# Performance work log

Measured on AMD Instinct MI355X. Metric: run time of the kernel, lower is better.

The kernel has to match this reference:

```python
import jax, jax.numpy as jnp
import numpy as np

B = 32        # graphs per batch
MAXN = 2048   # max nodes per graph (dense batch length)
HEADS = 8
DH = 64       # head dim (512/8)
M = 256       # FAVOR+ random features
D = 512
EPS = 1e-5    # batchnorm eps
KEPS = 1e-6   # performer stabilizer


def _batchnorm(x, g, b):
    # torch BatchNorm1d training-mode: biased batch statistics over node dim
    mu = jnp.mean(x, axis=0)
    var = jnp.mean((x - mu) ** 2, axis=0)
    return (x - mu) * jax.lax.rsqrt(var + EPS) * g + b


def setup_inputs() -> dict:
    key = jax.random.key(0)
    ks = jax.random.split(key, 10)
    sizes = 1024 + (np.arange(B) * 131) % 1025   # ragged graph sizes in [1024, 2048]
    N = int(sizes.sum())                          # 48544
    E = N * 8
    batch = jnp.asarray(np.repeat(np.arange(B), sizes), dtype=jnp.int32)
    edge_index = jax.random.randint(ks[0], (2, E), 0, N, dtype=jnp.int32)
    s = 1.0 / np.sqrt(D)
    return {
        'x': jax.random.normal(ks[1], (N, D), jnp.float32),
        'batch': batch,
        'edge_index': edge_index,
        'norm1_g': jnp.ones((D,), jnp.float32),
        'norm1_b': jnp.zeros((D,), jnp.float32),
        'norm2_g': jnp.ones((D,), jnp.float32),
        'norm2_b': jnp.zeros((D,), jnp.float32),
        'W_conv': jax.random.normal(ks[2], (D, D), jnp.float32) * s,
        'b_conv': jnp.zeros((D,), jnp.float32),
        'Wq': jax.random.normal(ks[3], (D, D), jnp.float32) * s,
        'Wk': jax.random.normal(ks[4], (D, D), jnp.float32) * s,
        'Wv': jax.random.normal(ks[5], (D, D), jnp.float32) * s,
        'Wo': jax.random.normal(ks[6], (D, D), jnp.float32) * s,
        'proj': jax.random.normal(ks[7], (M, DH), jnp.float32),
    }


def _forward(x, batch, edge_index, norm1_g, norm1_b, norm2_g, norm2_b,
             W_conv, b_conv, Wq, Wk, Wv, Wo, proj):
    N = x.shape[0]
    E = edge_index.shape[1]
    h = x

    # norm1 (+ dropout p=0 -> identity) then local GNN conv (mean-agg GCN + linear + relu)
    xn = _batchnorm(x, norm1_g, norm1_b)
    msg = xn[edge_index[0]]                                        # [E, D] gather
    agg = jax.ops.segment_sum(msg, edge_index[1], num_segments=N)  # [N, D] scatter-add
    deg = jax.ops.segment_sum(jnp.ones((E,), x.dtype), edge_index[1], num_segments=N)
    agg = agg / jnp.maximum(deg, 1.0)[:, None]
    conv_out = jax.nn.relu(agg @ W_conv + b_conv)

    # to_dense_batch(h, batch) -> h_dense [B, MAXN, D], mask [B, MAXN]
    counts = jax.ops.segment_sum(jnp.ones((N,), jnp.int32), batch, num_segments=B)
    offsets = jnp.concatenate([jnp.zeros((1,), jnp.int32), jnp.cumsum(counts)[:-1]])
    pos = jnp.arange(N, dtype=jnp.int32) - offsets[batch]
    h_dense = jnp.zeros((B, MAXN, D), x.dtype).at[batch, pos].set(h)
    mask = jnp.zeros((B, MAXN), bool).at[batch, pos].set(True)

    # Performer FAVOR+ non-causal self-attention
    def heads(t, W):
        return (t @ W).reshape(B, MAXN, HEADS, DH).transpose(0, 2, 1, 3)  # [B,H,MAXN,DH]
    q, k, v = heads(h_dense, Wq), heads(h_dense, Wk), heads(h_dense, Wv)

    scale = DH ** -0.25  # data normalizer applied to q and k each

    def phi(t, is_query):
        t = t * scale
        u = jnp.einsum('bhnd,md->bhnm', t, proj)           # [B,H,MAXN,M]
        diag = 0.5 * jnp.sum(t * t, axis=-1, keepdims=True)
        if is_query:
            m_ = jnp.max(u, axis=-1, keepdims=True)
        else:
            m_ = jnp.max(u, axis=(-2, -1), keepdims=True)
        return jnp.exp(u - diag - jax.lax.stop_gradient(m_)) / np.sqrt(M) + KEPS

    qf = phi(q, True)
    kf = phi(k, False) * mask[:, None, :, None]   # zero padded keys
    vm = v * mask[:, None, :, None]

    kv = jnp.einsum('bhnm,bhnd->bhmd', kf, vm)                    # [B,H,M,DH]
    z = 1.0 / (jnp.einsum('bhnm,bhm->bhn', qf, kf.sum(axis=2)) + KEPS)
    attn = jnp.einsum('bhnm,bhmd->bhnd', qf, kv) * z[..., None]   # [B,H,MAXN,DH]
    attn = attn.transpose(0, 2, 1, 3).reshape(B, MAXN, D) @ Wo

    h_attn = attn[batch, pos]                                      # gather back: [mask]

    return _batchnorm(conv_out + h_attn + h, norm2_g, norm2_b)


def reference(x, batch, edge_index, norm1_g, norm1_b, norm2_g, norm2_b,
              W_conv, b_conv, Wq, Wk, Wv, Wo, proj):
    return _forward(x, batch, edge_index, norm1_g, norm1_b, norm2_g, norm2_b,
                    W_conv, b_conv, Wq, Wk, Wv, Wo, proj)
```

## Files before the change

### kernel.cpp

```cpp
#include <hip/hip_runtime.h>
#include <stdint.h>

#define CDIV(a,b) (((a)+(b)-1)/(b))

typedef __attribute__((ext_vector_type(4))) float f32x4;
typedef __attribute__((ext_vector_type(8))) short s16x8;
typedef __attribute__((ext_vector_type(8))) unsigned short u16x8;
typedef __attribute__((ext_vector_type(4))) unsigned short u16x4;

__device__ __forceinline__ float bf2f(unsigned short u) {
  union { unsigned int i; float f; } c; c.i = ((unsigned int)u) << 16; return c.f;
}
__device__ __forceinline__ unsigned short f2bf(float f) {
  union { float f; unsigned int i; } c; c.f = f;
  unsigned int u = c.i;
  u += 0x7fffu + ((u >> 16) & 1u);
  return (unsigned short)(u >> 16);
}

template<int BM, int BN, int WM, int WN, int EPI>
__global__ __launch_bounds__(256) void gemm_bt(
    const unsigned short* __restrict__ A, const unsigned short* __restrict__ B,
    void* __restrict__ Cout, const float* __restrict__ aux,
    int K, int lda, int ldb, int ldc, long zsC, int Mstore)
{
  constexpr int MT = BM / (WM * 16);
  constexpr int NT = BN / (WN * 16);
  constexpr int LDT = 40;
  __shared__ unsigned short As[BM * LDT];
  __shared__ unsigned short Bs[BN * LDT];
  const int tid = threadIdx.x, wid = tid >> 6, lane = tid & 63;
  const int wr = wid / WN, wc = wid % WN;
  long m0 = (long)blockIdx.y * BM;
  const int n0 = blockIdx.x * BN;
  f32x4 acc[MT][NT] = {};
  for (int k0 = 0; k0 < K; k0 += 32) {
    #pragma unroll
    for (int c = tid; c < BM * 4; c += 256) {
      int row = c >> 2, c8 = (c & 3) * 8;
      *(u16x8*)(&As[row * LDT + c8]) = *(const u16x8*)(A + (m0 + row) * lda + k0 + c8);
    }
    #pragma unroll
    for (int c = tid; c < BN * 4; c += 256) {
      int row = c >> 2, c8 = (c & 3) * 8;
      *(u16x8*)(&Bs[row * LDT + c8]) = *(const u16x8*)(B + (long)(n0 + row) * ldb + k0 + c8);
    }
    __syncthreads();
    s16x8 af[MT], bfv[NT];
    #pragma unroll
    for (int mt = 0; mt < MT; mt++)
      af[mt] = *(const s16x8*)(&As[(wr * MT * 16 + mt * 16 + (lane & 15)) * LDT + ((lane >> 4) * 8)]);
    #pragma unroll
    for (int nt = 0; nt < NT; nt++)
      bfv[nt] = *(const s16x8*)(&Bs[(wc * NT * 16 + nt * 16 + (lane & 15)) * LDT + ((lane >> 4) * 8)]);
    #pragma unroll
    for (int mt = 0; mt < MT; mt++)
      #pragma unroll
      for (int nt = 0; nt < NT; nt++)
        acc[mt][nt] = __builtin_amdgcn_mfma_f32_16x16x32_bf16(af[mt], bfv[nt], acc[mt][nt], 0, 0, 0);
    __syncthreads();
  }
  #pragma unroll
  for (int mt = 0; mt < MT; mt++) {
    const int rl0 = wr * (MT * 16) + mt * 16 + ((lane >> 4) << 2);
    #pragma unroll
    for (int nt = 0; nt < NT; nt++) {
      const int col = n0 + wc * (NT * 16) + nt * 16 + (lane & 15);
      #pragma unroll
      for (int i = 0; i < 4; i++) {
        long r = m0 + rl0 + i;
        if (r < Mstore) {
          float v = acc[mt][nt][i];
          long ci = r * ldc + col;
          if constexpr (EPI == 5) {
            float o = v + aux[col];
            o = o > 0.f ? o : 0.f;
            ((float*)Cout)[ci] += o;
          } else if constexpr (EPI == 7) {
            ((unsigned short*)Cout)[(long)(col >> 6) * zsC + r * 64 + (col & 63)] = f2bf(v);
          } else if constexpr (EPI == 8) {
            ((float*)Cout)[ci] = v + aux[ci];
          }
        }
      }
    }
  }
}

__global__ __launch_bounds__(256) void k_kmax(
    const unsigned short* __restrict__ kvqh, const unsigned short* __restrict__ projb,
    const unsigned int* __restrict__ offs, unsigned int* __restrict__ kmax, long Npad) {
  __shared__ float wmax[4];
  const int tid = threadIdx.x, wid = tid >> 6, lane = tid & 63;
  const int b = blockIdx.y, h = blockIdx.z;
  const unsigned int off = offs[b];
  const int nb = (int)(offs[b + 1] - off);
  const int m0 = blockIdx.x * 64;
  if (m0 >= nb) return;
  const unsigned short* A = kvqh + ((long)(8 + h) * Npad + off + m0) * 64;
  f32x4 acc[4][4] = {};
  #pragma unroll
  for (int k0 = 0; k0 < 64; k0 += 32) {
    s16x8 af[4], bfv[4];
    #pragma unroll
    for (int mt = 0; mt < 4; mt++)
      af[mt] = *(const s16x8*)(A + (long)(mt * 16 + (lane & 15)) * 64 + k0 + ((lane >> 4) * 8));
    #pragma unroll
    for (int nt = 0; nt < 4; nt++)
      bfv[nt] = *(const s16x8*)(projb + (long)(wid * 64 + nt * 16 + (lane & 15)) * 64 + k0 + ((lane >> 4) * 8));
    #pragma unroll
    for (int mt = 0; mt < 4; mt++)
      #pragma unroll
      for (int nt = 0; nt < 4; nt++)
        acc[mt][nt] = __builtin_amdgcn_mfma_f32_16x16x32_bf16(af[mt], bfv[nt], acc[mt][nt], 0, 0, 0);
  }
  float bm = -3.0e38f;
  #pragma unroll
  for (int mt = 0; mt < 4; mt++)
    #pragma unroll
    for (int i = 0; i < 4; i++) {
      int row = mt * 16 + ((lane >> 4) << 2) + i;
      if (m0 + row < nb) {
        #pragma unroll
        for (int nt = 0; nt < 4; nt++) bm = fmaxf(bm, acc[mt][nt][i]);
      }
    }
  #pragma unroll
  for (int s = 1; s < 64; s <<= 1) bm = fmaxf(bm, __shfl_xor(bm, s));
  if (lane == 0) wmax[wid] = bm;
  __syncthreads();
  if (tid == 0) {
    float m = fmaxf(fmaxf(wmax[0], wmax[1]), fmaxf(wmax[2], wmax[3]));
    atomicMax(&kmax[b * 8 + h], __float_as_uint(fmaxf(m, 0.f)));
  }
}

__global__ __launch_bounds__(256) void k_kvm(
    const unsigned short* __restrict__ kvqh, const unsigned short* __restrict__ projb,
    const unsigned int* __restrict__ offs, const unsigned int* __restrict__ kmax,
    unsigned short* __restrict__ kvTb, float* __restrict__ kfsum, long Npad) {
  constexpr int TLD = 72;
  __shared__ unsigned short vsT[2][64 * TLD];
  __shared__ unsigned short kfsT[64 * TLD];
  const int tid = threadIdx.x, wid = tid >> 6, lane = tid & 63;
  const int mblk = blockIdx.x, b = blockIdx.y, h = blockIdx.z;
  const unsigned int off = offs[b];
  const int nb = (int)(offs[b + 1] - off);
  const float km = __uint_as_float(kmax[b * 8 + h]);
  const unsigned short* Kp = kvqh + ((long)(8 + h) * Npad + off) * 64;
  const unsigned short* Vp = kvqh + ((long)(16 + h) * Npad + off) * 64;
  const unsigned short* Pp = projb + (long)(mblk * 64 + wid * 16) * 64;
  const int l15 = lane & 15, hi = lane >> 4;
  const int mloc = wid * 16 + l15;

  #pragma unroll
  for (int c = tid; c < 512; c += 256) {
    int row = c >> 3, c8 = (c & 7) * 8;
    int rot = (c & 7) * 8;
    u16x8 v = *(const u16x8*)(Vp + (long)row * 64 + c8);
    #pragma unroll
    for (int j = 0; j < 8; j++) vsT[0][(c8 + j) * TLD + ((row + rot) & 63)] = v[j];
  }
  __syncthreads();

  f32x4 akv[4] = {};
  float ksum = 0.f;
  int buf = 0;
  for (int n0 = 0; n0 < nb; n0 += 64) {
    f32x4 acc[4] = {};
    float dsum[4] = {0.f, 0.f, 0.f, 0.f};
    #pragma unroll
    for (int k0 = 0; k0 < 64; k0 += 32) {
      s16x8 af[4];
      #pragma unroll
      for (int mt = 0; mt < 4; mt++)
        af[mt] = *(const s16x8*)(Kp + ((long)n0 + mt * 16 + l15) * 64 + k0 + hi * 8);
      s16x8 bfv = *(const s16x8*)(Pp + (long)l15 * 64 + k0 + hi * 8);
      #pragma unroll
      for (int mt = 0; mt < 4; mt++) {
        #pragma unroll
        for (int j = 0; j < 8; j++) {
          float a = bf2f((unsigned short)af[mt][j]);
          dsum[mt] += a * a;
        }
        acc[mt] = __builtin_amdgcn_mfma_f32_16x16x32_bf16(af[mt], bfv, acc[mt], 0, 0, 0);
      }
    }
    float rs[4];
    #pragma unroll
    for (int mt = 0; mt < 4; mt++) {
      float s = dsum[mt];
      s += __shfl_xor(s, 16); s += __shfl_xor(s, 32);
      rs[mt] = 0.0625f * s;
    }
    #pragma unroll
    for (int mt = 0; mt < 4; mt++) {
      int r0 = mt * 16 + hi * 4;
      float e[4];
      #pragma unroll
      for (int i = 0; i < 4; i++) {
        float dg = __shfl(rs[mt], hi * 4 + i);
        e[i] = (n0 + r0 + i < nb) ? (__expf(acc[mt][i] - dg - km) * 0.0625f + 1e-6f) : 0.f;
      }
      ksum += e[0] + e[1] + e[2] + e[3];
      unsigned int p0 = (unsigned int)f2bf(e[0]) | ((unsigned int)f2bf(e[1]) << 16);
      unsigned int p1 = (unsigned int)f2bf(e[2]) | ((unsigned int)f2bf(e[3]) << 16);
      *(unsigned int*)(&kfsT[mloc * TLD + r0]) = p0;
      *(unsigned int*)(&kfsT[mloc * TLD + r0 + 2]) = p1;
    }
    if (n0 + 64 < nb) {
      #pragma unroll
      for (int c = tid; c < 512; c += 256) {
        int row = c >> 3, c8 = (c & 7) * 8;
        int rot = (c & 7) * 8;
        u16x8 v = *(const u16x8*)(Vp + ((long)n0 + 64 + row) * 64 + c8);
        #pragma unroll
        for (int j = 0; j < 8; j++) vsT[buf ^ 1][(c8 + j) * TLD + ((row + rot) & 63)] = v[j];
      }
    }
    #pragma unroll
    for (int ks = 0; ks < 2; ks++) {
      s16x8 bB = *(const s16x8*)(&kfsT[mloc * TLD + ks * 32 + hi * 8]);
      #pragma unroll
      for (int mt2 = 0; mt2 < 4; mt2++) {
        int d = mt2 * 16 + l15;
        int rrot = ((ks * 32 + hi * 8) + ((d >> 3) & 7) * 8) & 63;
        s16x8 aA = *(const s16x8*)(&vsT[buf][d * TLD + rrot]);
        akv[mt2] = __builtin_amdgcn_mfma_f32_16x16x32_bf16(aA, bB, akv[mt2], 0, 0, 0);
      }
    }
    __syncthreads();
    buf ^= 1;
  }
  long base = ((long)b * 8 + h) * 16384;
  const int m = mblk * 64 + mloc;
  #pragma unroll
  for (int mt2 = 0; mt2 < 4; mt2++)
    #pragma unroll
    for (int i = 0; i < 4; i++) {
      int d = mt2 * 16 + hi * 4 + i;
      kvTb[base + (long)d * 256 + m] = f2bf(akv[mt2][i]);
    }
  ksum += __shfl_xor(ksum, 16); ksum += __shfl_xor(ksum, 32);
  if (hi == 0) kfsum[((long)b * 8 + h) * 256 + m] = ksum;
}

__global__ __launch_bounds__(256) void k_qflash(
    const unsigned short* __restrict__ qh_all, const unsigned short* __restrict__ projb,
    const unsigned short* __restrict__ kvTb, const float* __restrict__ kfsum,
    const unsigned int* __restrict__ offs, unsigned short* __restrict__ attn, long Npad) {
  constexpr int QLDT = 264;
  __shared__ unsigned short qfs[64 * QLDT];
  __shared__ float skf[256];
  __shared__ float sdiag[64];
  __shared__ float smax[4][64];
  __shared__ float szp[4][64];
  const int tid = threadIdx.x, wid = tid >> 6, lane = tid & 63;
  const int b = blockIdx.y, h = blockIdx.z;
  const unsigned int off = offs[b];
  const int nb = (int)(offs[b + 1] - off);
  const int m0 = blockIdx.x * 64;
  if (m0 >= nb) return;
  const unsigned short* A = qh_all + ((long)h * Npad + off + m0) * 64;
  skf[tid] = kfsum[((long)b * 8 + h) * 256 + tid];
  f32x4 acc[4][4] = {};
  float dsum[4] = {0.f, 0.f, 0.f, 0.f};
  #pragma unroll
  for (int k0 = 0; k0 < 64; k0 += 32) {
    s16x8 af[4], bfv[4];
    #pragma unroll
    for (int mt = 0; mt < 4; mt++)
      af[mt] = *(const s16x8*)(A + (long)(mt * 16 + (lane & 15)) * 64 + k0 + ((lane >> 4) * 8));
    #pragma unroll
    for (int nt = 0; nt < 4; nt++)
      bfv[nt] = *(const s16x8*)(projb + (long)(wid * 64 + nt * 16 + (lane & 15)) * 64 + k0 + ((lane >> 4) * 8));
    if (wid == 0) {
      #pragma unroll
      for (int mt = 0; mt < 4; mt++)
        #pragma unroll
        for (int j = 0; j < 8; j++) {
          float a = bf2f((unsigned short)af[mt][j]);
          dsum[mt] += a * a;
        }
    }
    #pragma unroll
    for (int mt = 0; mt < 4; mt++)
      #pragma unroll
      for (int nt = 0; nt < 4; nt++)
        acc[mt][nt] = __builtin_amdgcn_mfma_f32_16x16x32_bf16(af[mt], bfv[nt], acc[mt][nt], 0, 0, 0);
  }
  if (wid == 0) {
    #pragma unroll
    for (int mt = 0; mt < 4; mt++) {
      float s = dsum[mt];
      s += __shfl_xor(s, 16); s += __shfl_xor(s, 32);
      if (lane < 16) sdiag[mt * 16 + lane] = 0.0625f * s;
    }
  }
  #pragma unroll
  for (int mt = 0; mt < 4; mt++)
    #pragma unroll
    for (int i = 0; i < 4; i++) {
      float rm = fmaxf(fmaxf(acc[mt][0][i], acc[mt][1][i]), fmaxf(acc[mt][2][i], acc[mt][3][i]));
      rm = fmaxf(rm, __shfl_xor(rm, 1)); rm = fmaxf(rm, __shfl_xor(rm, 2));
      rm = fmaxf(rm, __shfl_xor(rm, 4)); rm = fmaxf(rm, __shfl_xor(rm, 8));
      if ((lane & 15) == 0) smax[wid][mt * 16 + ((lane >> 4) << 2) + i] = rm;
    }
  __syncthreads();
  #pragma unroll
  for (int mt = 0; mt < 4; mt++)
    #pragma unroll
    for (int i = 0; i < 4; i++) {
      int row = mt * 16 + ((lane >> 4) << 2) + i;
      float rm = fmaxf(fmaxf(smax[0][row], smax[1][row]), fmaxf(smax[2][row], smax[3][row]));
      float dg = sdiag[row];
      float zp = 0.f;
      #pragma unroll
      for (int nt = 0; nt < 4; nt++) {
        int col = wid * 64 + nt * 16 + (lane & 15);
        float e = __expf(acc[mt][nt][i] - dg - rm) * 0.0625f + 1e-6f;
        qfs[row * QLDT + col] = f2bf(e);
        zp += e * skf[col];
      }
      zp += __shfl_xor(zp, 1); zp += __shfl_xor(zp, 2);
      zp += __shfl_xor(zp, 4); zp += __shfl_xor(zp, 8);
      if ((lane & 15) == 0) szp[wid][row] = zp;
    }
  __syncthreads();
  const unsigned short* kvb = kvTb + ((long)b * 8 + h) * 16384;
  f32x4 acc2[4] = {};
  #pragma unroll
  for (int ks = 0; ks < 8; ks++) {
    s16x8 aq = *(const s16x8*)(&qfs[(wid * 16 + (lane & 15)) * QLDT + ks * 32 + ((lane >> 4) * 8)]);
    #pragma unroll
    for (int ntd = 0; ntd < 4; ntd++) {
      s16x8 bk = *(const s16x8*)(kvb + (long)(ntd * 16 + (lane & 15)) * 256 + ks * 32 + ((lane >> 4) * 8));
      acc2[ntd] = __builtin_amdgcn_mfma_f32_16x16x32_bf16(aq, bk, acc2[ntd], 0, 0, 0);
    }
  }
  #pragma unroll
  for (int ntd = 0; ntd < 4; ntd++)
    #pragma unroll
    for (int i = 0; i < 4; i++) {
      int row = wid * 16 + ((lane >> 4) << 2) + i;
      if (m0 + row < nb) {
        float zr = 1.f / (szp[0][row] + szp[1][row] + szp[2][row] + szp[3][row] + 1e-6f);
        attn[(long)(off + m0 + row) * 512 + h * 64 + ntd * 16 + (lane & 15)] = f2bf(acc2[ntd][i] * zr);
      }
    }
}


__global__ void k_fill(float* __restrict__ out, long n, float v) {
  long i = (long)blockIdx.x * 256 + threadIdx.x;
  if (i < n) out[i] = v;
}

__global__ void k_convert_x(const float* __restrict__ x, unsigned short* __restrict__ xb,
                            long ntotal, long nreal) {
  long i = ((long)blockIdx.x * 256 + threadIdx.x) * 4;
  if (i >= ntotal) return;
  u16x4 o;
  if (i < nreal) {
    f32x4 v = *(const f32x4*)(x + i);
    o[0] = f2bf(v[0]); o[1] = f2bf(v[1]); o[2] = f2bf(v[2]); o[3] = f2bf(v[3]);
  } else { o[0] = 0; o[1] = 0; o[2] = 0; o[3] = 0; }
  *(u16x4*)(xb + i) = o;
}

__global__ void k_transall(const float* __restrict__ w0, const float* __restrict__ w1,
                           const float* __restrict__ w2, const float* __restrict__ w3,
                           const float* __restrict__ w4, unsigned short* __restrict__ out) {
  long idx = (long)blockIdx.x * 256 + threadIdx.x;
  if (idx >= (5L << 18)) return;
  int which = (int)(idx >> 18);
  int r = (int)(idx & 262143);
  int n = r >> 9, k = r & 511;
  const float* w = which == 0 ? w0 : which == 1 ? w1 : which == 2 ? w2 : which == 3 ? w3 : w4;
  out[idx] = f2bf(w[k * 512 + n]);
}

__global__ void k_scale_copy_bf(const float* __restrict__ in, unsigned short* __restrict__ out,
                                int n, float scl) {
  int i = blockIdx.x * 256 + threadIdx.x;
  if (i < n) out[i] = f2bf(in[i] * scl);
}

__global__ void k_bn_stats(const float* __restrict__ x, float* __restrict__ s1,
                           float* __restrict__ s2, int N, int rpb) {
  int t = threadIdx.x;
  int r0 = blockIdx.x * rpb;
  int r1 = min(N, r0 + rpb);
  float a1 = 0, a2 = 0, b1 = 0, b2 = 0;
  for (int r = r0; r < r1; r++) {
    float va = x[(long)r * 512 + t];
    float vb = x[(long)r * 512 + t + 256];
    a1 += va; a2 += va * va; b1 += vb; b2 += vb * vb;
  }
  atomicAdd(&s1[t], a1); atomicAdd(&s2[t], a2);
  atomicAdd(&s1[t + 256], b1); atomicAdd(&s2[t + 256], b2);
}

__global__ void k_bn_final(const float* __restrict__ s1, const float* __restrict__ s2,
                           const float* __restrict__ g, const float* __restrict__ b,
                           float* __restrict__ a, float* __restrict__ c, float invN) {
  int t = threadIdx.x;
  float mu = s1[t] * invN;
  float var = s2[t] * invN - mu * mu;
  float inv = rsqrtf(var + 1e-5f);
  float av = g[t] * inv;
  a[t] = av;
  c[t] = b[t] - mu * av;
}

__global__ void k_deg(const int* __restrict__ ed, unsigned int* __restrict__ deg, long E) {
  long i = (long)blockIdx.x * 256 + threadIdx.x;
  if (i < E) atomicAdd(&deg[ed[i]], 1u);
}

__global__ void k_offs(const int* __restrict__ batch, unsigned int* __restrict__ offs, int N) {
  int i = blockIdx.x * 256 + threadIdx.x;
  if (i >= N) return;
  int b = batch[i];
  if (i == 0) { for (int bb = 0; bb <= b; bb++) offs[bb] = 0; }
  else {
    int pb = batch[i - 1];
    if (pb != b) for (int bb = pb + 1; bb <= b; bb++) offs[bb] = i;
  }
  if (i == N - 1) { for (int bb = b + 1; bb <= 32; bb++) offs[bb] = N; }
}

__global__ __launch_bounds__(1024) void k_scan_nodes(const unsigned int* __restrict__ deg,
                                                     unsigned int* __restrict__ rowstart, int N) {
  __shared__ unsigned int wsum[16];
  __shared__ unsigned int carry_s;
  int t = threadIdx.x, lane = t & 63, wid = t >> 6;
  if (t == 0) carry_s = 0;
  __syncthreads();
  for (int base = 0; base < N; base += 1024) {
    int i = base + t;
    unsigned int v = (i < N) ? deg[i] : 0;
    unsigned int sc = v;
    #pragma unroll
    for (int s = 1; s < 64; s <<= 1) {
      unsigned int u = __shfl_up(sc, s);
      if (lane >= s) sc += u;
    }
    if (lane == 63) wsum[wid] = sc;
    __syncthreads();
    unsigned int woff = 0, tot = 0;
    #pragma unroll
    for (int w = 0; w < 16; w++) { unsigned int s = wsum[w]; if (w < wid) woff += s; tot += s; }
    unsigned int carry = carry_s;
    if (i < N) rowstart[i] = carry + woff + sc - v;
    __syncthreads();
    if (t == 0) carry_s = carry + tot;
    __syncthreads();
  }
  if (threadIdx.x == 0) rowstart[N] = carry_s;
}

__global__ void k_csr_fill(const int* __restrict__ es, const int* __restrict__ ed,
                           const unsigned int* __restrict__ rowstart,
                           unsigned int* __restrict__ cursor, int* __restrict__ csr, long E) {
  long e = (long)blockIdx.x * 256 + threadIdx.x;
  if (e >= E) return;
  int d = ed[e];
  unsigned int slot = atomicAdd(&cursor[d], 1u);
  csr[rowstart[d] + slot] = es[e];
}

__global__ __launch_bounds__(128) void k_gather(const int* __restrict__ csr,
                                                const unsigned int* __restrict__ rowstart,
                                                const float* __restrict__ x,
                                                const float* __restrict__ a1, const float* __restrict__ c1,
                                                unsigned short* __restrict__ conv_in, int N) {
  long n = blockIdx.x;
  int c = threadIdx.x * 4;
  u16x4 o; o[0] = 0; o[1] = 0; o[2] = 0; o[3] = 0;
  if (n < N) {
    unsigned int r0 = rowstart[n], r1 = rowstart[n + 1];
    if (r1 > r0) {
      f32x4 acc0 = {}, acc1 = {};
      unsigned int j = r0;
      for (; j + 2 <= r1; j += 2) {
        int s0 = csr[j], s1 = csr[j + 1];
        acc0 += *(const f32x4*)(x + (long)s0 * 512 + c);
        acc1 += *(const f32x4*)(x + (long)s1 * 512 + c);
      }
      if (j < r1) { int s0 = csr[j]; acc0 += *(const f32x4*)(x + (long)s0 * 512 + c); }
      f32x4 acc = acc0 + acc1;
      float inv = 1.f / (float)(r1 - r0);
      o[0] = f2bf(acc[0] * inv * a1[c + 0] + c1[c + 0]);
      o[1] = f2bf(acc[1] * inv * a1[c + 1] + c1[c + 1]);
      o[2] = f2bf(acc[2] * inv * a1[c + 2] + c1[c + 2]);
      o[3] = f2bf(acc[3] * inv * a1[c + 3] + c1[c + 3]);
    }
  }
  *(u16x4*)(conv_in + n * 512 + c) = o;
}

__global__ void k_stats(const float* __restrict__ y, float* __restrict__ s1,
                        float* __restrict__ s2, int N, int rpb) {
  int t = threadIdx.x;
  int r0 = blockIdx.x * rpb;
  int r1 = min(N, r0 + rpb);
  float a1 = 0, a2 = 0, b1 = 0, b2 = 0;
  for (int r = r0; r < r1; r++) {
    float va = y[(long)r * 512 + t];
    float vb = y[(long)r * 512 + t + 256];
    a1 += va; a2 += va * va; b1 += vb; b2 += vb * vb;
  }
  atomicAdd(&s1[t], a1); atomicAdd(&s2[t], a2);
  atomicAdd(&s1[t + 256], b1); atomicAdd(&s2[t + 256], b2);
}

__global__ void k_bn_apply(float* __restrict__ y, const float* __restrict__ a,
                           const float* __restrict__ c, long total) {
  long i4 = ((long)blockIdx.x * 256 + threadIdx.x) * 4;
  if (i4 >= total) return;
  int col = (int)(i4 & 511);
  f32x4 v = *(const f32x4*)(y + i4);
  #pragma unroll
  for (int j = 0; j < 4; j++) v[j] = v[j] * a[col + j] + c[col + j];
  *(f32x4*)(y + i4) = v;
}


extern "C" void kernel_launch(void* const* d_in, const int* in_sizes, int n_in,
                              void* d_out, int out_size, void* d_ws, size_t ws_size,
                              hipStream_t stream) {
  (void)n_in; (void)out_size;
  const float* x = (const float*)d_in[0];
  const int* batch = (const int*)d_in[1];
  const int* eidx = (const int*)d_in[2];
  const float* n1g = (const float*)d_in[3];
  const float* n1b = (const float*)d_in[4];
  const float* n2g = (const float*)d_in[5];
  const float* n2b = (const float*)d_in[6];
  const float* wconv = (const float*)d_in[7];
  const float* bconv = (const float*)d_in[8];
  const float* wq = (const float*)d_in[9];
  const float* wk = (const float*)d_in[10];
  const float* wv = (const float*)d_in[11];
  const float* wo = (const float*)d_in[12];
  const float* proj = (const float*)d_in[13];

  const int N = in_sizes[1];
  const long E = in_sizes[2] / 2;
  const long Npad = CDIV(N, 128) * 128 + 256;
  const int Mb = (int)((CDIV(N, 128) * 128 + 128) / 128);
  const int* es = eidx;
  const int* ed = eidx + E;
  float* out = (float*)d_out;

  char* p = (char*)d_ws;
  auto alloc = [&](size_t bytes) -> char* {
    char* r = p;
    p += (bytes + 255) & ~(size_t)255;
    return r;
  };
  unsigned short* kvqh = (unsigned short*)alloc((size_t)24 * Npad * 64 * 2);
  unsigned short* xbf  = (unsigned short*)alloc((size_t)Npad * 512 * 2);
  unsigned short* kvT_b = (unsigned short*)alloc((size_t)32 * 8 * 16384 * 2);
  unsigned short* wts   = (unsigned short*)alloc((size_t)5 * 512 * 512 * 2);
  unsigned short* proj_s = (unsigned short*)alloc((size_t)256 * 64 * 2);
  float* bn1_acc = (float*)alloc(1024 * 4);
  float* bn1_ac  = (float*)alloc(1024 * 4);
  float* bn2_acc = (float*)alloc(1024 * 4);
  float* bn2_ac  = (float*)alloc(1024 * 4);
  unsigned int* deg      = (unsigned int*)alloc((size_t)N * 4);
  unsigned int* offs     = (unsigned int*)alloc(33 * 4);
  unsigned int* kmax     = (unsigned int*)alloc(32 * 8 * 4);
  float* kfsum = (float*)alloc((size_t)32 * 8 * 256 * 4);
  unsigned int* rowstart = (unsigned int*)alloc((size_t)(N + 1) * 4);
  unsigned int* cursor   = (unsigned int*)alloc((size_t)N * 4);
  int* csr               = (int*)alloc((size_t)E * 4);
  size_t required = (size_t)(p - (char*)d_ws);
  if (required > ws_size) {
    k_fill<<<(int)CDIV((long)N * 512, 256), 256, 0, stream>>>(
        out, (long)N * 512, 1.0e6f + (float)(ws_size >> 20));
    return;
  }
  unsigned short* wqkv_t  = wts;
  unsigned short* wconv_t = wts + 3 * 512 * 512;
  unsigned short* wo_t    = wts + 4 * 512 * 512;
  unsigned short* attn_all = xbf;
  unsigned short* conv_in  = xbf;

  hipMemsetAsync(deg, 0, (size_t)N * 4, stream);
  hipMemsetAsync(cursor, 0, (size_t)N * 4, stream);
  hipMemsetAsync(kmax, 0, 32 * 8 * 4, stream);
  hipMemsetAsync(bn1_acc, 0, 1024 * 4, stream);
  hipMemsetAsync(bn2_acc, 0, 1024 * 4, stream);

  k_convert_x<<<(int)CDIV(Npad * 512 / 4, 256), 256, 0, stream>>>(x, xbf, Npad * 512, (long)N * 512);
  k_transall<<<(int)CDIV(5L << 18, 256), 256, 0, stream>>>(wq, wk, wv, wconv, wo, wts);
  k_scale_copy_bf<<<CDIV(256 * 64, 256), 256, 0, stream>>>(proj, proj_s, 256 * 64, 0.35355339059327373f);

  int rpb = CDIV(N, 1024);
  k_bn_stats<<<1024, 256, 0, stream>>>(x, bn1_acc, bn1_acc + 512, N, rpb);
  k_bn_final<<<1, 512, 0, stream>>>(bn1_acc, bn1_acc + 512, n1g, n1b, bn1_ac, bn1_ac + 512, 1.f / N);
  k_deg<<<(int)CDIV(E, 256), 256, 0, stream>>>(ed, deg, E);
  k_offs<<<CDIV(N, 256), 256, 0, stream>>>(batch, offs, N);
  k_scan_nodes<<<1, 1024, 0, stream>>>(deg, rowstart, N);
  k_csr_fill<<<(int)CDIV(E, 256), 256, 0, stream>>>(es, ed, rowstart, cursor, csr, E);

  gemm_bt<128, 128, 2, 2, 7><<<dim3(12, Mb), 256, 0, stream>>>(
      xbf, wqkv_t, kvqh, nullptr, 512, 512, 512, 0, (long)Npad * 64, (int)Npad);

  k_kmax<<<dim3(32, 32, 8), 256, 0, stream>>>(kvqh, proj_s, offs, kmax, Npad);
  k_kvm<<<dim3(4, 32, 8), 256, 0, stream>>>(kvqh, proj_s, offs, kmax, kvT_b, kfsum, Npad);

  k_qflash<<<dim3(32, 32, 8), 256, 0, stream>>>(
      kvqh, proj_s, kvT_b, kfsum, offs, attn_all, Npad);

  gemm_bt<128, 128, 2, 2, 8><<<dim3(4, Mb), 256, 0, stream>>>(
      attn_all, wo_t, out, x, 512, 512, 512, 512, 0, N);

  k_gather<<<(int)(CDIV(N, 128) * 128), 128, 0, stream>>>(csr, rowstart, x, bn1_ac, bn1_ac + 512, conv_in, N);
  gemm_bt<128, 128, 2, 2, 5><<<dim3(4, Mb), 256, 0, stream>>>(
      conv_in, wconv_t, out, bconv, 512, 512, 512, 512, 0, N);

  k_stats<<<1024, 256, 0, stream>>>(out, bn2_acc, bn2_acc + 512, N, rpb);
  k_bn_final<<<1, 512, 0, stream>>>(bn2_acc, bn2_acc + 512, n2g, n2b, bn2_ac, bn2_ac + 512, 1.f / N);
  k_bn_apply<<<(int)CDIV((long)N * 512 / 4, 256), 256, 0, stream>>>(out, bn2_ac, bn2_ac + 512, (long)N * 512);
}
```

Before: 1.187 ms.

## Fuse x conversion with BN stats, fold key-sum into kv MFMA, reorder grids

The x-to-bf16 conversion now runs in the same pass as the first batchnorm statistics, so x is read once instead of twice. The separate padding-zero pass becomes a memset. The performer normaliser is computed by an extra MFMA against a key-feature-sum row stored in bf16 alongside kv, which removes the shared-memory dot product and the cross-wave reduction in k_qflash. The attention grids are flattened so that batch/head varies fastest, and the QKV GEMM uses 256-wide N tiles. Storing the key sum in bf16 costs precision in the denominator, and an extra memset clears the enlarged kv buffer.

```diff
diff --git a/kernel.cpp b/kernel.cpp
--- a/kernel.cpp
+++ b/kernel.cpp
@@ -17,6 +17,8 @@
   u += 0x7fffu + ((u >> 16) & 1u);
   return (unsigned short)(u >> 16);
 }
+
+#define KVROWS 80
 
 template<int BM, int BN, int WM, int WN, int EPI>
 __global__ __launch_bounds__(256) void gemm_bt(
@@ -92,10 +94,11 @@
     const unsigned int* __restrict__ offs, unsigned int* __restrict__ kmax, long Npad) {
   __shared__ float wmax[4];
   const int tid = threadIdx.x, wid = tid >> 6, lane = tid & 63;
-  const int b = blockIdx.y, h = blockIdx.z;
+  const int bh = blockIdx.x & 255, xb = blockIdx.x >> 8;
+  const int b = bh >> 3, h = bh & 7;
   const unsigned int off = offs[b];
   const int nb = (int)(offs[b + 1] - off);
-  const int m0 = blockIdx.x * 64;
+  const int m0 = xb * 64;
   if (m0 >= nb) return;
   const unsigned short* A = kvqh + ((long)(8 + h) * Npad + off + m0) * 64;
   f32x4 acc[4][4] = {};
@@ -138,12 +141,13 @@
 __global__ __launch_bounds__(256) void k_kvm(
     const unsigned short* __restrict__ kvqh, const unsigned short* __restrict__ projb,
     const unsigned int* __restrict__ offs, const unsigned int* __restrict__ kmax,
-    unsigned short* __restrict__ kvTb, float* __restrict__ kfsum, long Npad) {
+    unsigned short* __restrict__ kvTb, long Npad) {
   constexpr int TLD = 72;
   __shared__ unsigned short vsT[2][64 * TLD];
   __shared__ unsigned short kfsT[64 * TLD];
   const int tid = threadIdx.x, wid = tid >> 6, lane = tid & 63;
-  const int mblk = blockIdx.x, b = blockIdx.y, h = blockIdx.z;
+  const int bh = blockIdx.x & 255, mblk = blockIdx.x >> 8;
+  const int b = bh >> 3, h = bh & 7;
   const unsigned int off = offs[b];
   const int nb = (int)(offs[b + 1] - off);
   const float km = __uint_as_float(kmax[b * 8 + h]);
@@ -232,7 +236,7 @@
     __syncthreads();
     buf ^= 1;
   }
-  long base = ((long)b * 8 + h) * 16384;
+  long base = ((long)b * 8 + h) * (KVROWS * 256);
   const int m = mblk * 64 + mloc;
   #pragma unroll
   for (int mt2 = 0; mt2 < 4; mt2++)
@@ -242,27 +246,26 @@
       kvTb[base + (long)d * 256 + m] = f2bf(akv[mt2][i]);
     }
   ksum += __shfl_xor(ksum, 16); ksum += __shfl_xor(ksum, 32);
-  if (hi == 0) kfsum[((long)b * 8 + h) * 256 + m] = ksum;
+  if (hi == 0) kvTb[base + 64 * 256 + m] = f2bf(ksum);
 }
 
 __global__ __launch_bounds__(256) void k_qflash(
     const unsigned short* __restrict__ qh_all, const unsigned short* __restrict__ projb,
-    const unsigned short* __restrict__ kvTb, const float* __restrict__ kfsum,
-    const unsigned int* __restrict__ offs, unsigned short* __restrict__ attn, long Npad) {
+    const unsigned short* __restrict__ kvTb, const unsigned int* __restrict__ offs,
+    unsigned short* __restrict__ attn, long Npad) {
   constexpr int QLDT = 264;
   __shared__ unsigned short qfs[64 * QLDT];
-  __shared__ float skf[256];
   __shared__ float sdiag[64];
   __shared__ float smax[4][64];
-  __shared__ float szp[4][64];
   const int tid = threadIdx.x, wid = tid >> 6, lane = tid & 63;
-  const int b = blockIdx.y, h = blockIdx.z;
+  const int l15 = lane & 15, hi = lane >> 4;
+  const int bh = blockIdx.x & 255, xb = blockIdx.x >> 8;
+  const int b = bh >> 3, h = bh & 7;
   const unsigned int off = offs[b];
   const int nb = (int)(offs[b + 1] - off);
-  const int m0 = blockIdx.x * 64;
+  const int m0 = xb * 64;
   if (m0 >= nb) return;
   const unsigned short* A = qh_all + ((long)h * Npad + off + m0) * 64;
-  skf[tid] = kfsum[((long)b * 8 + h) * 256 + tid];
   f32x4 acc[4][4] = {};
   float dsum[4] = {0.f, 0.f, 0.f, 0.f};
   #pragma unroll
@@ -270,10 +273,10 @@
     s16x8 af[4], bfv[4];
     #pragma unroll
     for (int mt = 0; mt < 4; mt++)
-      af[mt] = *(const s16x8*)(A + (long)(mt * 16 + (lane & 15)) * 64 + k0 + ((lane >> 4) * 8));
+      af[mt] = *(const s16x8*)(A + (long)(mt * 16 + l15) * 64 + k0 + hi * 8);
     #pragma unroll
     for (int nt = 0; nt < 4; nt++)
-      bfv[nt] = *(const s16x8*)(projb + (long)(wid * 64 + nt * 16 + (lane & 15)) * 64 + k0 + ((lane >> 4) * 8));
+      bfv[nt] = *(const s16x8*)(projb + (long)(wid * 64 + nt * 16 + l15) * 64 + k0 + hi * 8);
     if (wid == 0) {
       #pragma unroll
       for (int mt = 0; mt < 4; mt++)
@@ -304,49 +307,50 @@
       float rm = fmaxf(fmaxf(acc[mt][0][i], acc[mt][1][i]), fmaxf(acc[mt][2][i], acc[mt][3][i]));
       rm = fmaxf(rm, __shfl_xor(rm, 1)); rm = fmaxf(rm, __shfl_xor(rm, 2));
       rm = fmaxf(rm, __shfl_xor(rm, 4)); rm = fmaxf(rm, __shfl_xor(rm, 8));
-      if ((lane & 15) == 0) smax[wid][mt * 16 + ((lane >> 4) << 2) + i] = rm;
+      if (l15 == 0) smax[wid][mt * 16 + hi * 4 + i] = rm;
     }
   __syncthreads();
   #pragma unroll
   for (int mt = 0; mt < 4; mt++)
     #pragma unroll
     for (int i = 0; i < 4; i++) {
-      int row = mt * 16 + ((lane >> 4) << 2) + i;
+      int row = mt * 16 + hi * 4 + i;
       float rm = fmaxf(fmaxf(smax[0][row], smax[1][row]), fmaxf(smax[2][row], smax[3][row]));
-      float dg = sdiag[row];
-      float zp = 0.f;
+      float sub = sdiag[row] + rm;
       #pragma unroll
       for (int nt = 0; nt < 4; nt++) {
-        int col = wid * 64 + nt * 16 + (lane & 15);
-        float e = __expf(acc[mt][nt][i] - dg - rm) * 0.0625f + 1e-6f;
-        qfs[row * QLDT + col] = f2bf(e);
-        zp += e * skf[col];
-      }
-      zp += __shfl_xor(zp, 1); zp += __shfl_xor(zp, 2);
-      zp += __shfl_xor(zp, 4); zp += __shfl_xor(zp, 8);
-      if ((lane & 15) == 0) szp[wid][row] = zp;
+        int col = wid * 64 + nt * 16 + l15;
+        qfs[row * QLDT + col] = f2bf(__expf(acc[mt][nt][i] - sub) * 0.0625f + 1e-6f);
+      }
     }
   __syncthreads();
-  const unsigned short* kvb = kvTb + ((long)b * 8 + h) * 16384;
+  const unsigned short* kvb = kvTb + ((long)b * 8 + h) * (KVROWS * 256);
   f32x4 acc2[4] = {};
+  f32x4 acc3 = {};
   #pragma unroll
   for (int ks = 0; ks < 8; ks++) {
-    s16x8 aq = *(const s16x8*)(&qfs[(wid * 16 + (lane & 15)) * QLDT + ks * 32 + ((lane >> 4) * 8)]);
-    #pragma unroll
-    for (int ntd = 0; ntd < 4; ntd++) {
-      s16x8 bk = *(const s16x8*)(kvb + (long)(ntd * 16 + (lane & 15)) * 256 + ks * 32 + ((lane >> 4) * 8));
-      acc2[ntd] = __builtin_amdgcn_mfma_f32_16x16x32_bf16(aq, bk, acc2[ntd], 0, 0, 0);
-    }
-  }
-  #pragma unroll
-  for (int ntd = 0; ntd < 4; ntd++)
+    s16x8 aq = *(const s16x8*)(&qfs[(wid * 16 + l15) * QLDT + ks * 32 + hi * 8]);
+    #pragma unroll
+    for (int t = 0; t < 4; t++) {
+      s16x8 bk = *(const s16x8*)(kvb + (long)(t * 16 + l15) * 256 + ks * 32 + hi * 8);
+      acc2[t] = __builtin_amdgcn_mfma_f32_16x16x32_bf16(aq, bk, acc2[t], 0, 0, 0);
+    }
+    s16x8 bz = *(const s16x8*)(kvb + (long)(64 + l15) * 256 + ks * 32 + hi * 8);
+    acc3 = __builtin_amdgcn_mfma_f32_16x16x32_bf16(aq, bz, acc3, 0, 0, 0);
+  }
+  float zr[4];
+  #pragma unroll
+  for (int i = 0; i < 4; i++) {
+    float zden = __shfl(acc3[i], hi * 16);
+    zr[i] = 1.f / (zden + 1e-6f);
+  }
+  #pragma unroll
+  for (int t = 0; t < 4; t++)
     #pragma unroll
     for (int i = 0; i < 4; i++) {
-      int row = wid * 16 + ((lane >> 4) << 2) + i;
-      if (m0 + row < nb) {
-        float zr = 1.f / (szp[0][row] + szp[1][row] + szp[2][row] + szp[3][row] + 1e-6f);
-        attn[(long)(off + m0 + row) * 512 + h * 64 + ntd * 16 + (lane & 15)] = f2bf(acc2[ntd][i] * zr);
-      }
+      int row = wid * 16 + hi * 4 + i;
+      if (m0 + row < nb)
+        attn[(long)(off + m0 + row) * 512 + h * 64 + t * 16 + l15] = f2bf(acc2[t][i] * zr[i]);
     }
 }
 
@@ -356,16 +360,21 @@
   if (i < n) out[i] = v;
 }
 
-__global__ void k_convert_x(const float* __restrict__ x, unsigned short* __restrict__ xb,
-                            long ntotal, long nreal) {
-  long i = ((long)blockIdx.x * 256 + threadIdx.x) * 4;
-  if (i >= ntotal) return;
-  u16x4 o;
-  if (i < nreal) {
-    f32x4 v = *(const f32x4*)(x + i);
-    o[0] = f2bf(v[0]); o[1] = f2bf(v[1]); o[2] = f2bf(v[2]); o[3] = f2bf(v[3]);
-  } else { o[0] = 0; o[1] = 0; o[2] = 0; o[3] = 0; }
-  *(u16x4*)(xb + i) = o;
+__global__ void k_convx_stats(const float* __restrict__ x, unsigned short* __restrict__ xb,
+                              float* __restrict__ s1, float* __restrict__ s2, int N, int rpb) {
+  int t = threadIdx.x;
+  int r0 = blockIdx.x * rpb;
+  int r1 = min(N, r0 + rpb);
+  float a1 = 0, a2 = 0, b1 = 0, b2 = 0;
+  for (int r = r0; r < r1; r++) {
+    const float* xr = x + (long)r * 512 + 2 * t;
+    float va = xr[0], vb = xr[1];
+    a1 += va; a2 += va * va; b1 += vb; b2 += vb * vb;
+    *(unsigned int*)(xb + (long)r * 512 + 2 * t) =
+        (unsigned int)f2bf(va) | ((unsigned int)f2bf(vb) << 16);
+  }
+  atomicAdd(&s1[2 * t], a1); atomicAdd(&s2[2 * t], a2);
+  atomicAdd(&s1[2 * t + 1], b1); atomicAdd(&s2[2 * t + 1], b2);
 }
 
 __global__ void k_transall(const float* __restrict__ w0, const float* __restrict__ w1,
@@ -384,21 +393,6 @@
                                 int n, float scl) {
   int i = blockIdx.x * 256 + threadIdx.x;
   if (i < n) out[i] = f2bf(in[i] * scl);
-}
-
-__global__ void k_bn_stats(const float* __restrict__ x, float* __restrict__ s1,
-                           float* __restrict__ s2, int N, int rpb) {
-  int t = threadIdx.x;
-  int r0 = blockIdx.x * rpb;
-  int r1 = min(N, r0 + rpb);
-  float a1 = 0, a2 = 0, b1 = 0, b2 = 0;
-  for (int r = r0; r < r1; r++) {
-    float va = x[(long)r * 512 + t];
-    float vb = x[(long)r * 512 + t + 256];
-    a1 += va; a2 += va * va; b1 += vb; b2 += vb * vb;
-  }
-  atomicAdd(&s1[t], a1); atomicAdd(&s2[t], a2);
-  atomicAdd(&s1[t + 256], b1); atomicAdd(&s2[t + 256], b2);
 }
 
 __global__ void k_bn_final(const float* __restrict__ s1, const float* __restrict__ s2,
@@ -562,7 +556,7 @@
   };
   unsigned short* kvqh = (unsigned short*)alloc((size_t)24 * Npad * 64 * 2);
   unsigned short* xbf  = (unsigned short*)alloc((size_t)Npad * 512 * 2);
-  unsigned short* kvT_b = (unsigned short*)alloc((size_t)32 * 8 * 16384 * 2);
+  unsigned short* kvT_b = (unsigned short*)alloc((size_t)32 * 8 * KVROWS * 256 * 2);
   unsigned short* wts   = (unsigned short*)alloc((size_t)5 * 512 * 512 * 2);
   unsigned short* proj_s = (unsigned short*)alloc((size_t)256 * 64 * 2);
   float* bn1_acc = (float*)alloc(1024 * 4);
@@ -572,7 +566,6 @@
   unsigned int* deg      = (unsigned int*)alloc((size_t)N * 4);
   unsigned int* offs     = (unsigned int*)alloc(33 * 4);
   unsigned int* kmax     = (unsigned int*)alloc(32 * 8 * 4);
-  float* kfsum = (float*)alloc((size_t)32 * 8 * 256 * 4);
   unsigned int* rowstart = (unsigned int*)alloc((size_t)(N + 1) * 4);
   unsigned int* cursor   = (unsigned int*)alloc((size_t)N * 4);
   int* csr               = (int*)alloc((size_t)E * 4);
@@ -593,27 +586,27 @@
   hipMemsetAsync(kmax, 0, 32 * 8 * 4, stream);
   hipMemsetAsync(bn1_acc, 0, 1024 * 4, stream);
   hipMemsetAsync(bn2_acc, 0, 1024 * 4, stream);
-
-  k_convert_x<<<(int)CDIV(Npad * 512 / 4, 256), 256, 0, stream>>>(x, xbf, Npad * 512, (long)N * 512);
+  hipMemsetAsync(kvT_b, 0, (size_t)32 * 8 * KVROWS * 256 * 2, stream);
+  hipMemsetAsync(xbf + (size_t)N * 512, 0, (size_t)(Npad - N) * 512 * 2, stream);
+
+  int rpb = CDIV(N, 1024);
+  k_convx_stats<<<1024, 256, 0, stream>>>(x, xbf, bn1_acc, bn1_acc + 512, N, rpb);
   k_transall<<<(int)CDIV(5L << 18, 256), 256, 0, stream>>>(wq, wk, wv, wconv, wo, wts);
   k_scale_copy_bf<<<CDIV(256 * 64, 256), 256, 0, stream>>>(proj, proj_s, 256 * 64, 0.35355339059327373f);
-
-  int rpb = CDIV(N, 1024);
-  k_bn_stats<<<1024, 256, 0, stream>>>(x, bn1_acc, bn1_acc + 512, N, rpb);
   k_bn_final<<<1, 512, 0, stream>>>(bn1_acc, bn1_acc + 512, n1g, n1b, bn1_ac, bn1_ac + 512, 1.f / N);
   k_deg<<<(int)CDIV(E, 256), 256, 0, stream>>>(ed, deg, E);
   k_offs<<<CDIV(N, 256), 256, 0, stream>>>(batch, offs, N);
   k_scan_nodes<<<1, 1024, 0, stream>>>(deg, rowstart, N);
   k_csr_fill<<<(int)CDIV(E, 256), 256, 0, stream>>>(es, ed, rowstart, cursor, csr, E);
 
-  gemm_bt<128, 128, 2, 2, 7><<<dim3(12, Mb), 256, 0, stream>>>(
+  gemm_bt<128, 256, 2, 2, 7><<<dim3(6, Mb), 256, 0, stream>>>(
       xbf, wqkv_t, kvqh, nullptr, 512, 512, 512, 0, (long)Npad * 64, (int)Npad);
 
-  k_kmax<<<dim3(32, 32, 8), 256, 0, stream>>>(kvqh, proj_s, offs, kmax, Npad);
-  k_kvm<<<dim3(4, 32, 8), 256, 0, stream>>>(kvqh, proj_s, offs, kmax, kvT_b, kfsum, Npad);
-
-  k_qflash<<<dim3(32, 32, 8), 256, 0, stream>>>(
-      kvqh, proj_s, kvT_b, kfsum, offs, attn_all, Npad);
+  k_kmax<<<32 * 256, 256, 0, stream>>>(kvqh, proj_s, offs, kmax, Npad);
+  k_kvm<<<4 * 256, 256, 0, stream>>>(kvqh, proj_s, offs, kmax, kvT_b, Npad);
+
+  k_qflash<<<32 * 256, 256, 0, stream>>>(
+      kvqh, proj_s, kvT_b, offs, attn_all, Npad);
 
   gemm_bt<128, 128, 2, 2, 8><<<dim3(4, Mb), 256, 0, stream>>>(
       attn_all, wo_t, out, x, 512, 512, 512, 512, 0, N);
```

Measured after the change: 1.326 ms. 11.7% more time.
